# Optimization experiments

Hardware: AMD Instinct MI355X
Metric: run time of the kernel (lower is better)

The kernel has to match this reference:

```python
import jax, jax.numpy as jnp
import numpy as np

D_MODEL = 256
N_LAYER = 8
N_HEAD = 8
D_K = D_MODEL // N_HEAD  # 32
D_FF = 4 * D_MODEL
VOCAB = 5
NUM_BUCKETS = 64
MAX_DIST = 256
L = 768
B = 1
EPS = 1e-5


def _ln(x, s, b):
    m = jnp.mean(x, axis=-1, keepdims=True)
    v = jnp.mean((x - m) ** 2, axis=-1, keepdims=True)
    return (x - m) * jax.lax.rsqrt(v + EPS) * s + b


def _rp_bucket(rel_pos):
    # faithful to RelativePositionBias._relative_position_bucket
    nb = NUM_BUCKETS // 2  # 32
    ret = (rel_pos < 0).astype(jnp.int32) * nb
    arp = jnp.abs(rel_pos)
    max_exact = nb // 2  # 16
    is_small = arp < max_exact
    safe = jnp.maximum(arp, 1).astype(jnp.float32)
    log_ratio = float(np.log(MAX_DIST / max_exact))
    vil = max_exact + (jnp.log(safe / max_exact) / log_ratio * (nb - max_exact)).astype(jnp.int32)
    vil = jnp.minimum(vil, nb - 1)
    return ret + jnp.where(is_small, arp.astype(jnp.int32), vil)


def setup_inputs() -> dict:
    key = jax.random.key(0)
    ks = iter(jax.random.split(key, 40))
    s = 0.02
    d = {}
    d['seq'] = jax.random.randint(next(ks), (B, L), 0, VOCAB, dtype=jnp.int32)
    d['tok_emb'] = jax.random.normal(next(ks), (VOCAB, D_MODEL), jnp.float32) * s
    d['rp_emb'] = jax.random.normal(next(ks), (NUM_BUCKETS, N_HEAD), jnp.float32) * s
    # stacked per-layer params [N_LAYER, ...]
    d['wq'] = jax.random.normal(next(ks), (N_LAYER, D_MODEL, D_MODEL), jnp.float32) * s
    d['wk'] = jax.random.normal(next(ks), (N_LAYER, D_MODEL, D_MODEL), jnp.float32) * s
    d['wv'] = jax.random.normal(next(ks), (N_LAYER, D_MODEL, D_MODEL), jnp.float32) * s
    d['wo'] = jax.random.normal(next(ks), (N_LAYER, D_MODEL, D_MODEL), jnp.float32) * s
    d['ln1_s'] = jnp.ones((N_LAYER, D_MODEL), jnp.float32)
    d['ln1_b'] = jnp.zeros((N_LAYER, D_MODEL), jnp.float32)
    d['ln2_s'] = jnp.ones((N_LAYER, D_MODEL), jnp.float32)
    d['ln2_b'] = jnp.zeros((N_LAYER, D_MODEL), jnp.float32)
    d['ffn_w1'] = jax.random.normal(next(ks), (N_LAYER, D_MODEL, D_FF), jnp.float32) * s
    d['ffn_b1'] = jnp.zeros((N_LAYER, D_FF), jnp.float32)
    d['ffn_w2'] = jax.random.normal(next(ks), (N_LAYER, D_FF, D_MODEL), jnp.float32) * s
    d['ffn_b2'] = jnp.zeros((N_LAYER, D_MODEL), jnp.float32)
    d['lnf_s'] = jnp.ones((D_MODEL,), jnp.float32)
    d['lnf_b'] = jnp.zeros((D_MODEL,), jnp.float32)
    d['pair_q_w'] = jax.random.normal(next(ks), (D_MODEL, D_MODEL), jnp.float32) * s
    d['pair_q_b'] = jnp.zeros((D_MODEL,), jnp.float32)
    d['pair_k_w'] = jax.random.normal(next(ks), (D_MODEL, D_MODEL), jnp.float32) * s
    d['pair_k_b'] = jnp.zeros((D_MODEL,), jnp.float32)
    d['pair_rp_emb'] = jax.random.normal(next(ks), (NUM_BUCKETS, D_MODEL), jnp.float32) * s
    d['cls_w1'] = jax.random.normal(next(ks), (D_MODEL, D_MODEL), jnp.float32) * s
    d['cls_b1'] = jnp.zeros((D_MODEL,), jnp.float32)
    d['cls_w2'] = jax.random.normal(next(ks), (D_MODEL, 2), jnp.float32) * s
    d['cls_b2'] = jnp.zeros((2,), jnp.float32)
    return d


def reference(seq, tok_emb, rp_emb, wq, wk, wv, wo, ln1_s, ln1_b, ln2_s, ln2_b,
              ffn_w1, ffn_b1, ffn_w2, ffn_b2, lnf_s, lnf_b,
              pair_q_w, pair_q_b, pair_k_w, pair_k_b, pair_rp_emb,
              cls_w1, cls_b1, cls_w2, cls_b2):
    scale = D_K ** 0.5
    x = tok_emb[seq]  # [B, L, D]
    pos = jnp.arange(L)
    rel = pos[:, None] - pos[None, :]  # [L, L]
    bucket = _rp_bucket(rel)  # [L, L] int32
    bias = jnp.transpose(rp_emb[bucket], (2, 0, 1))[None]  # [1, H, L, L]

    def step(x, p):
        Wq, Wk, Wv, Wo, s1, b1, s2, b2, fw1, fb1, fw2, fb2 = p
        h = _ln(x, s1, b1)
        q = (h @ Wq).reshape(B, L, N_HEAD, D_K).transpose(0, 2, 1, 3)
        k = (h @ Wk).reshape(B, L, N_HEAD, D_K).transpose(0, 2, 1, 3)
        v = (h @ Wv).reshape(B, L, N_HEAD, D_K).transpose(0, 2, 1, 3)
        attn = jnp.einsum('bhid,bhjd->bhij', q / scale, k) + bias
        attn = jax.nn.softmax(attn, axis=-1)
        o = jnp.einsum('bhij,bhjd->bhid', attn, v)
        o = o.transpose(0, 2, 1, 3).reshape(B, L, D_MODEL) @ Wo
        x = x + o
        h2 = _ln(x, s2, b2)
        f = jax.nn.gelu(h2 @ fw1 + fb1, approximate=False) @ fw2 + fb2
        return x + f, None

    x, _ = jax.lax.scan(step, x, (wq, wk, wv, wo, ln1_s, ln1_b, ln2_s, ln2_b,
                                  ffn_w1, ffn_b1, ffn_w2, ffn_b2))
    x = _ln(x, lnf_s, lnf_b)
    q = x @ pair_q_w + pair_q_b  # [B, L, D]
    k = x @ pair_k_w + pair_k_b
    px = jnp.einsum('bic,bjc->bijc', q, k)  # [B, L, L, D]
    px = px + pair_rp_emb[bucket][None]  # add [L, L, D] pair rel-pos embedding
    px = jax.nn.relu(px @ cls_w1 + cls_b1) @ cls_w2 + cls_b2  # [B, L, L, 2]
    return px
```

## Files before the change

kernel.cpp:

```cpp
#include <hip/hip_runtime.h>
#include <hip/hip_bf16.h>
#include <stdint.h>

#define LSEQ 768
#define DM   256
#define NH   8
#define DK   32
#define DFF  1024
#define NLAYER 8
#define NDD  1535

typedef __attribute__((ext_vector_type(8))) short     bf16x8;
typedef __attribute__((ext_vector_type(8))) _Float16  f16x8;
typedef __attribute__((ext_vector_type(4))) float     f32x4;

__device__ __forceinline__ unsigned short f2bf(float f) {
  unsigned u = __float_as_uint(f);
  u += 0x7fffu + ((u >> 16) & 1u);
  return (unsigned short)(u >> 16);
}
__device__ __forceinline__ unsigned short f2h(float f) {
  union { _Float16 h; unsigned short s; } c;
  c.h = (_Float16)f;
  return c.s;
}
__device__ __forceinline__ unsigned pk2(float a, float b) {
  __hip_bfloat162 h = __float22bfloat162_rn(make_float2(a, b));
  union { __hip_bfloat162 h; unsigned u; } c; c.h = h;
  return c.u;
}
__device__ __forceinline__ int bucket_of(int dd) {
  int rel = dd - 767;
  int ret = rel < 0 ? 32 : 0;
  int arp = rel < 0 ? -rel : rel;
  if (arp < 16) return ret + arp;
  const float lr = 2.772588722239781f;
  float val = logf((float)arp * 0.0625f) / lr * 16.0f;
  int vi = 16 + (int)val;
  return ret + (vi < 31 ? vi : 31);
}

__device__ __forceinline__ void pack8h(unsigned short* dst, int id,
                                       const float* src, int N, int G) {
  int lane = (id >> 3) & 63;
  int rem = id >> 9;
  int g = rem % G, kc = rem / G;
  int kb = kc * 32 + ((lane >> 4) << 3);
  int n = g * 16 + (lane & 15);
  union { unsigned short s[8]; uint4 v; } U;
  #pragma unroll
  for (int e = 0; e < 8; ++e) U.s[e] = f2h(src[(size_t)(kb + e) * N + n]);
  *(uint4*)(dst + id) = U.v;
}

__device__ __forceinline__ void pack8h_cat(unsigned short* dst, int id,
                                           const float* s0, const float* s1,
                                           const float* s2, int G) {
  int lane = (id >> 3) & 63;
  int rem = id >> 9;
  int g = rem % G, kc = rem / G;
  int kb = kc * 32 + ((lane >> 4) << 3);
  int n = g * 16 + (lane & 15);
  const float* sp = n < 256 ? s0 : (n < 512 ? s1 : s2);
  int nn = n & 255;
  union { unsigned short s[8]; uint4 v; } U;
  #pragma unroll
  for (int e = 0; e < 8; ++e) U.s[e] = f2h(sp[(size_t)(kb + e) * 256 + nn]);
  *(uint4*)(dst + id) = U.v;
}

template <int LN, int GR>
__device__ void gemm_tile(const float* gsrc, const int* seqIdx,
                          const float* B, const float* bias, float* C,
                          const float* lns, const float* lnb,
                          int M, int K, int N, int m0, int n0, char* smc) {
  float (*As)[32][68] = (float (*)[32][68])smc;
  float (*Bs)[32][68] = (float (*)[32][68])(smc + 17408);
  float (*stat)[2]    = (float (*)[2])(smc + 34816);
  float (*red)[8]     = (float (*)[8])(smc + 35328);

  int t = threadIdx.x;
  int arow = t >> 2, akq = (t & 3) * 8;
  int mg = m0 + arow;
  int mgc = mg < M ? mg : M - 1;
  const float* Ar = (GR == 1) ? (gsrc + (size_t)seqIdx[mgc] * K)
                              : (gsrc + (size_t)bucket_of(mgc) * K);
  float mean = 0.f, rstd = 0.f;
  if (LN) {
    int lq = t & 3;
    float s = 0.f, s2 = 0.f;
    const float* p = Ar + lq * 64;
    #pragma unroll
    for (int c = 0; c < 64; c += 4) {
      float4 v = *(const float4*)(p + c);
      s  += v.x + v.y + v.z + v.w;
      s2 += v.x * v.x + v.y * v.y + v.z * v.z + v.w * v.w;
    }
    red[arow][lq] = s; red[arow][lq + 4] = s2;
    __syncthreads();
    if (lq == 0) {
      float sm = red[arow][0] + red[arow][1] + red[arow][2] + red[arow][3];
      float sq = red[arow][4] + red[arow][5] + red[arow][6] + red[arow][7];
      float m = sm * (1.f / 256.f);
      float v = sq * (1.f / 256.f) - m * m;
      stat[arow][0] = m;
      stat[arow][1] = rsqrtf(v + 1e-5f);
    }
    __syncthreads();
    mean = stat[arow][0]; rstd = stat[arow][1];
  }

  int bkr = t >> 3, bn8 = (t & 7) * 8;
  int ty = t >> 4, tx = t & 15;
  float acc[4][4] = {};
  int nk = K >> 5;

  for (int kt = 0; kt < nk; ++kt) {
    int k0 = kt << 5;
    float4 a0 = *(const float4*)(Ar + k0 + akq);
    float4 a1 = *(const float4*)(Ar + k0 + akq + 4);
    if (LN) {
      float4 ls0 = *(const float4*)(lns + k0 + akq), ls1 = *(const float4*)(lns + k0 + akq + 4);
      float4 lb0 = *(const float4*)(lnb + k0 + akq), lb1 = *(const float4*)(lnb + k0 + akq + 4);
      a0.x=(a0.x-mean)*rstd*ls0.x+lb0.x; a0.y=(a0.y-mean)*rstd*ls0.y+lb0.y;
      a0.z=(a0.z-mean)*rstd*ls0.z+lb0.z; a0.w=(a0.w-mean)*rstd*ls0.w+lb0.w;
      a1.x=(a1.x-mean)*rstd*ls1.x+lb1.x; a1.y=(a1.y-mean)*rstd*ls1.y+lb1.y;
      a1.z=(a1.z-mean)*rstd*ls1.z+lb1.z; a1.w=(a1.w-mean)*rstd*ls1.w+lb1.w;
    }
    int cur = kt & 1;
    As[cur][akq+0][arow]=a0.x; As[cur][akq+1][arow]=a0.y; As[cur][akq+2][arow]=a0.z; As[cur][akq+3][arow]=a0.w;
    As[cur][akq+4][arow]=a1.x; As[cur][akq+5][arow]=a1.y; As[cur][akq+6][arow]=a1.z; As[cur][akq+7][arow]=a1.w;
    *(float4*)&Bs[cur][bkr][bn8] = *(const float4*)(B + (size_t)(k0 + bkr) * N + n0 + bn8);
    *(float4*)&Bs[cur][bkr][bn8+4] = *(const float4*)(B + (size_t)(k0 + bkr) * N + n0 + bn8 + 4);
    __syncthreads();
    #pragma unroll 8
    for (int kk = 0; kk < 32; ++kk) {
      float4 a = *(float4*)&As[cur][kk][ty * 4];
      float4 b = *(float4*)&Bs[cur][kk][tx * 4];
      acc[0][0]=fmaf(a.x,b.x,acc[0][0]); acc[0][1]=fmaf(a.x,b.y,acc[0][1]);
      acc[0][2]=fmaf(a.x,b.z,acc[0][2]); acc[0][3]=fmaf(a.x,b.w,acc[0][3]);
      acc[1][0]=fmaf(a.y,b.x,acc[1][0]); acc[1][1]=fmaf(a.y,b.y,acc[1][1]);
      acc[1][2]=fmaf(a.y,b.z,acc[1][2]); acc[1][3]=fmaf(a.y,b.w,acc[1][3]);
      acc[2][0]=fmaf(a.z,b.x,acc[2][0]); acc[2][1]=fmaf(a.z,b.y,acc[2][1]);
      acc[2][2]=fmaf(a.z,b.z,acc[2][2]); acc[2][3]=fmaf(a.z,b.w,acc[2][3]);
      acc[3][0]=fmaf(a.w,b.x,acc[3][0]); acc[3][1]=fmaf(a.w,b.y,acc[3][1]);
      acc[3][2]=fmaf(a.w,b.z,acc[3][2]); acc[3][3]=fmaf(a.w,b.w,acc[3][3]);
    }
    __syncthreads();
  }

  #pragma unroll
  for (int u = 0; u < 4; ++u) {
    int m = m0 + ty * 4 + u;
    if (m < M) {
      int n = n0 + tx * 4;
      float4 val = make_float4(acc[u][0], acc[u][1], acc[u][2], acc[u][3]);
      if (bias) {
        float4 bv = *(const float4*)(bias + n);
        val.x += bv.x; val.y += bv.y; val.z += bv.z; val.w += bv.w;
      }
      *(float4*)(C + (size_t)m * N + n) = val;
    }
  }
}

__global__ __launch_bounds__(256, 2) void k_prep(
    const int* __restrict__ seq, const float* __restrict__ tok_emb,
    const float* __restrict__ rp_emb,
    const float* __restrict__ wq, const float* __restrict__ wk,
    const float* __restrict__ wv, const float* __restrict__ wo,
    const float* __restrict__ ffn_w1, const float* __restrict__ ffn_w2,
    const float* __restrict__ ln1s0, const float* __restrict__ ln1b0,
    const float* __restrict__ pair_rp, const float* __restrict__ cls_w1,
    const float* __restrict__ cls_b1,
    const float* __restrict__ pair_q_w, const float* __restrict__ pair_k_w,
    float* x0, float* q0, float* k0, float* v0, float* RB,
    unsigned short* W1p, float* abias,
    unsigned short* Wop, unsigned short* W1pk, unsigned short* W2pk,
    unsigned short* Wqkvp, unsigned short* Wpairp) {
  __shared__ __align__(16) char sm[37376];
  int b = blockIdx.x, t = threadIdx.x;
  if (b < 96) {
    int m0 = (b % 24) * 64, n0 = (b / 24) * 64;
    gemm_tile<0,2>(pair_rp, nullptr, cls_w1, cls_b1, RB,
                   nullptr, nullptr, NDD, 256, 256, m0, n0, sm);
  } else if (b < 240) {
    int u = b - 96;
    int n0g = (u % 12) * 64, m0 = (u / 12) * 64;
    int bi = n0g >> 8, n0 = n0g & 255;
    const float* B = bi == 0 ? wq : (bi == 1 ? wk : wv);
    float* C = bi == 0 ? q0 : (bi == 1 ? k0 : v0);
    gemm_tile<1,1>(tok_emb, seq, B, nullptr, C,
                   ln1s0, ln1b0, LSEQ, 256, 256, m0, n0, sm);
  } else if (b < 432) {
    int row = (b - 240) * 4 + (t >> 6), c = (t & 63) * 4;
    *(float4*)(x0 + (size_t)row * DM + c) =
        *(const float4*)(tok_emb + (size_t)seq[row] * DM + c);
  } else if (b < 438) {
    int dd = (b - 432) * 256 + t;
    if (dd < NDD) {
      int bk = bucket_of(dd);
      #pragma unroll
      for (int h = 0; h < NH; ++h) abias[dd * 8 + h] = rp_emb[bk * 8 + h];
    }
  } else if (b < 502) {
    int base = (b - 438) * 1024 + t * 4;
    #pragma unroll
    for (int uu = 0; uu < 4; ++uu) {
      int id = base + uu;
      int e = id & 7, lane = (id >> 3) & 63, g = (id >> 9) & 15, kc = id >> 13;
      int kg = kc * 32 + (lane >> 4) * 8 + e;
      int n  = g * 16 + (lane & 15);
      W1p[id] = f2bf(cls_w1[(size_t)kg * 256 + n]);
    }
  } else {
    int u = (b - 502) * 2048 + t * 8;
    if (u < 524288) {
      int layer = u >> 16, id = u & 65535;
      pack8h(Wop + ((size_t)layer << 16), id, wo + ((size_t)layer << 16), 256, 16);
    } else if (u < 2621440) {
      int v2 = u - 524288; int layer = v2 >> 18, id = v2 & 262143;
      pack8h(W1pk + ((size_t)layer << 18), id, ffn_w1 + ((size_t)layer << 18), 1024, 64);
    } else if (u < 4718592) {
      int v2 = u - 2621440; int layer = v2 >> 18, id = v2 & 262143;
      pack8h(W2pk + ((size_t)layer << 18), id, ffn_w2 + ((size_t)layer << 18), 256, 16);
    } else if (u < 6291456) {
      int v2 = u - 4718592; int layer = v2 / 196608, id = v2 - layer * 196608;
      pack8h_cat(Wqkvp + (size_t)layer * 196608, id,
                 wq + ((size_t)layer << 16), wk + ((size_t)layer << 16),
                 wv + ((size_t)layer << 16), 48);
    } else {
      int id = u - 6291456;
      pack8h_cat(Wpairp, id, pair_q_w, pair_k_w, pair_k_w, 32);
    }
  }
}

#define ATTN_SMEM 72960

__global__ __launch_bounds__(256, 2) void k_attn2(
    const float* __restrict__ q, const float* __restrict__ k,
    const float* __restrict__ v, const float* __restrict__ abias,
    float* __restrict__ o) {
  extern __shared__ char sm[];
  float* S  = (float*)sm;
  float* KV = (float*)(sm + 49664);
  float* QS = (float*)(sm + 66560);
  float* BS = (float*)(sm + 68672);
  float (*red)[16] = (float (*)[16])(sm + 71808);
  float* mrow = (float*)(sm + 72832);
  float* linv = (float*)(sm + 72896);

  int i0 = blockIdx.x * 16, h = blockIdx.y, hc = h * DK;
  int t = threadIdx.x;

  for (int u = t; u < 783; u += 256)
    BS[u] = abias[(size_t)(i0 + u) * 8 + h];
  {
    int r = t >> 4, c = t & 15;
    const float inv = 0.17677669529663687f;
    QS[r * 33 + c]      = q[(size_t)(i0 + r) * DM + hc + c] * inv;
    QS[r * 33 + c + 16] = q[(size_t)(i0 + r) * DM + hc + c + 16] * inv;
  }

  int kx = t & 31, ry = t >> 5;
  int key = t >> 1, half = t & 1;

  for (int cc = 0; cc < 6; ++cc) {
    const float* kp = k + (size_t)(cc * 128 + key) * DM + hc + half * 16;
    float4 L0 = *(const float4*)(kp);
    float4 L1 = *(const float4*)(kp + 4);
    float4 L2 = *(const float4*)(kp + 8);
    float4 L3 = *(const float4*)(kp + 12);
    __syncthreads();
    int cb = half * 16;
    KV[(cb+ 0)*132+key]=L0.x; KV[(cb+ 1)*132+key]=L0.y; KV[(cb+ 2)*132+key]=L0.z; KV[(cb+ 3)*132+key]=L0.w;
    KV[(cb+ 4)*132+key]=L1.x; KV[(cb+ 5)*132+key]=L1.y; KV[(cb+ 6)*132+key]=L1.z; KV[(cb+ 7)*132+key]=L1.w;
    KV[(cb+ 8)*132+key]=L2.x; KV[(cb+ 9)*132+key]=L2.y; KV[(cb+10)*132+key]=L2.z; KV[(cb+11)*132+key]=L2.w;
    KV[(cb+12)*132+key]=L3.x; KV[(cb+13)*132+key]=L3.y; KV[(cb+14)*132+key]=L3.z; KV[(cb+15)*132+key]=L3.w;
    __syncthreads();

    float s0x=0,s0y=0,s0z=0,s0w=0, s1x=0,s1y=0,s1z=0,s1w=0;
    #pragma unroll
    for (int kk = 0; kk < 32; ++kk) {
      float q0 = QS[(ry*2    )*33 + kk];
      float q1 = QS[(ry*2 + 1)*33 + kk];
      float4 kv4 = *(const float4*)&KV[kk*132 + kx*4];
      s0x = fmaf(q0, kv4.x, s0x); s0y = fmaf(q0, kv4.y, s0y);
      s0z = fmaf(q0, kv4.z, s0z); s0w = fmaf(q0, kv4.w, s0w);
      s1x = fmaf(q1, kv4.x, s1x); s1y = fmaf(q1, kv4.y, s1y);
      s1z = fmaf(q1, kv4.z, s1z); s1w = fmaf(q1, kv4.w, s1w);
    }
    int jb = cc * 128 + kx * 4;
    int r0 = ry * 2, r1 = r0 + 1;
    S[r0*776 + jb+0] = s0x + BS[r0 + 767 - (jb+0)];
    S[r0*776 + jb+1] = s0y + BS[r0 + 767 - (jb+1)];
    S[r0*776 + jb+2] = s0z + BS[r0 + 767 - (jb+2)];
    S[r0*776 + jb+3] = s0w + BS[r0 + 767 - (jb+3)];
    S[r1*776 + jb+0] = s1x + BS[r1 + 767 - (jb+0)];
    S[r1*776 + jb+1] = s1y + BS[r1 + 767 - (jb+1)];
    S[r1*776 + jb+2] = s1z + BS[r1 + 767 - (jb+2)];
    S[r1*776 + jb+3] = s1w + BS[r1 + 767 - (jb+3)];
  }
  __syncthreads();

  {
    int ti = t >> 4, tj = t & 15;
    float mx = -1e30f;
    for (int jc = 0; jc < 48; ++jc)
      mx = fmaxf(mx, S[ti*776 + jc*16 + tj]);
    red[ti][tj] = mx;
    __syncthreads();
    if (tj == 0) {
      float m2 = red[ti][0];
      #pragma unroll
      for (int u = 1; u < 16; ++u) m2 = fmaxf(m2, red[ti][u]);
      mrow[ti] = m2;
    }
    __syncthreads();
    float m2 = mrow[ti];
    float sum = 0.f;
    for (int jc = 0; jc < 48; ++jc) {
      int j = jc*16 + tj;
      float e = __expf(S[ti*776 + j] - m2);
      S[ti*776 + j] = e;
      sum += e;
    }
    red[ti][tj] = sum;
    __syncthreads();
    if (tj == 0) {
      float s2 = 0.f;
      #pragma unroll
      for (int u = 0; u < 16; ++u) s2 += red[ti][u];
      linv[ti] = 1.f / s2;
    }
  }

  int cp = t & 15, jg = t >> 4;
  int c0 = cp * 2, c1 = c0 + 1;
  float oc0[16] = {}, oc1[16] = {};
  for (int cc = 0; cc < 6; ++cc) {
    const float* vp = v + (size_t)(cc * 128 + key) * DM + hc + half * 16;
    float4 L0 = *(const float4*)(vp);
    float4 L1 = *(const float4*)(vp + 4);
    float4 L2 = *(const float4*)(vp + 8);
    float4 L3 = *(const float4*)(vp + 12);
    __syncthreads();
    int cb = half * 16;
    KV[(cb+ 0)*132+key]=L0.x; KV[(cb+ 1)*132+key]=L0.y; KV[(cb+ 2)*132+key]=L0.z; KV[(cb+ 3)*132+key]=L0.w;
    KV[(cb+ 4)*132+key]=L1.x; KV[(cb+ 5)*132+key]=L1.y; KV[(cb+ 6)*132+key]=L1.z; KV[(cb+ 7)*132+key]=L1.w;
    KV[(cb+ 8)*132+key]=L2.x; KV[(cb+ 9)*132+key]=L2.y; KV[(cb+10)*132+key]=L2.z; KV[(cb+11)*132+key]=L2.w;
    KV[(cb+12)*132+key]=L3.x; KV[(cb+13)*132+key]=L3.y; KV[(cb+14)*132+key]=L3.z; KV[(cb+15)*132+key]=L3.w;
    __syncthreads();

    #pragma unroll
    for (int jj2 = 0; jj2 < 2; ++jj2) {
      int jb = jg * 8 + jj2 * 4;
      float4 vA = *(const float4*)&KV[c0*132 + jb];
      float4 vB = *(const float4*)&KV[c1*132 + jb];
      #pragma unroll
      for (int r = 0; r < 16; ++r) {
        float4 sv = *(const float4*)&S[r*776 + cc*128 + jb];
        oc0[r] += sv.x*vA.x + sv.y*vA.y + sv.z*vA.z + sv.w*vA.w;
        oc1[r] += sv.x*vB.x + sv.y*vB.y + sv.z*vB.z + sv.w*vB.w;
      }
    }
  }

  #pragma unroll
  for (int h2 = 0; h2 < 2; ++h2) {
    __syncthreads();
    #pragma unroll
    for (int r = 0; r < 8; ++r) {
      KV[(jg*8 + r)*32 + c0] = oc0[h2*8 + r];
      KV[(jg*8 + r)*32 + c1] = oc1[h2*8 + r];
    }
    __syncthreads();
    int r = t >> 5, c = t & 31;
    float s = 0.f;
    #pragma unroll
    for (int jgg = 0; jgg < 16; ++jgg) s += KV[(jgg*8 + r)*32 + c];
    o[(size_t)(i0 + h2*8 + r) * DM + hc + c] = s * linv[h2*8 + r];
  }
}


__global__ __launch_bounds__(256, 2) void k_t1(
    const float* __restrict__ o, const float* __restrict__ xin,
    const unsigned short* __restrict__ wop,
    const float* __restrict__ ln2s, const float* __restrict__ ln2b,
    const unsigned short* __restrict__ w1p, const float* __restrict__ fb1,
    float* __restrict__ x1, unsigned short* __restrict__ Fg) {
  __shared__ __align__(16) float    Xf[16][260];
  __shared__ __align__(16) _Float16 Ab[16][264];
  int t = threadIdx.x;
  int i0 = blockIdx.x * 16;
  int by = blockIdx.y;
  int w = t >> 6, l = t & 63;
  int lr = l & 15, lq = l >> 4;

  {
    int r = t >> 4, j = t & 15;
    #pragma unroll
    for (int q = 0; q < 4; ++q) {
      int c = j * 4 + q * 64;
      float4 v = *(const float4*)(o + (size_t)(i0 + r) * DM + c);
      union { _Float16 h[4]; uint2 u; } cv;
      cv.h[0] = (_Float16)v.x; cv.h[1] = (_Float16)v.y;
      cv.h[2] = (_Float16)v.z; cv.h[3] = (_Float16)v.w;
      *(uint2*)&Ab[r][c] = cv.u;
      *(float4*)&Xf[r][c] = *(const float4*)(xin + (size_t)(i0 + r) * DM + c);
    }
  }
  __syncthreads();

  f16x8 af[8];
  #pragma unroll
  for (int kc = 0; kc < 8; ++kc)
    af[kc] = *(const f16x8*)&Ab[lr][kc * 32 + lq * 8];

  {
    const unsigned short* wp = wop + (size_t)l * 8;
    #pragma unroll
    for (int gi = 0; gi < 4; ++gi) {
      int g = w * 4 + gi;
      f32x4 ac = {0.f, 0.f, 0.f, 0.f};
      #pragma unroll
      for (int kc = 0; kc < 8; ++kc) {
        f16x8 bb = *(const f16x8*)(wp + ((kc * 16 + g) << 9));
        ac = __builtin_amdgcn_mfma_f32_16x16x32_f16(af[kc], bb, ac, 0, 0, 0);
      }
      int n = g * 16 + lr;
      #pragma unroll
      for (int r = 0; r < 4; ++r)
        Xf[lq * 4 + r][n] += ac[r];
    }
  }
  __syncthreads();

  if (by == 0) {
    int r = t >> 4, j = t & 15;
    #pragma unroll
    for (int q = 0; q < 4; ++q) {
      int c = j * 4 + q * 64;
      *(float4*)(x1 + (size_t)(i0 + r) * DM + c) = *(const float4*)&Xf[r][c];
    }
  }

  {
    int r = t >> 4, j = t & 15;
    int c0 = j * 16;
    float xv[16]; float s1 = 0.f, s2 = 0.f;
    #pragma unroll
    for (int u = 0; u < 16; ++u) {
      xv[u] = Xf[r][c0 + u];
      s1 += xv[u]; s2 += xv[u] * xv[u];
    }
    #pragma unroll
    for (int m = 1; m < 16; m <<= 1) {
      s1 += __shfl_xor(s1, m);
      s2 += __shfl_xor(s2, m);
    }
    float mean = s1 * (1.f / 256.f);
    float var  = s2 * (1.f / 256.f) - mean * mean;
    float rs = rsqrtf(var + 1e-5f);
    #pragma unroll
    for (int p = 0; p < 4; ++p) {
      union { _Float16 h[4]; uint2 u; } cv;
      #pragma unroll
      for (int e = 0; e < 4; ++e) {
        int c = c0 + p * 4 + e;
        cv.h[e] = (_Float16)((xv[p * 4 + e] - mean) * rs * ln2s[c] + ln2b[c]);
      }
      *(uint2*)&Ab[r][c0 + p * 4] = cv.u;
    }
  }
  __syncthreads();

  #pragma unroll
  for (int kc = 0; kc < 8; ++kc)
    af[kc] = *(const f16x8*)&Ab[lr][kc * 32 + lq * 8];

  {
    const unsigned short* wp = w1p + (size_t)l * 8;
    #pragma unroll
    for (int gi = 0; gi < 4; ++gi) {
      int g = by * 16 + w * 4 + gi;
      f32x4 ac = {0.f, 0.f, 0.f, 0.f};
      #pragma unroll
      for (int kc = 0; kc < 8; ++kc) {
        f16x8 bb = *(const f16x8*)(wp + ((kc * 64 + g) << 9));
        ac = __builtin_amdgcn_mfma_f32_16x16x32_f16(af[kc], bb, ac, 0, 0, 0);
      }
      int n = g * 16 + lr;
      float b1 = fb1[n];
      #pragma unroll
      for (int r = 0; r < 4; ++r) {
        float v = ac[r] + b1;
        v = 0.5f * v * (1.f + erff(v * 0.70710678118654752f));
        Fg[(size_t)(i0 + lq * 4 + r) * DFF + n] = f2h(v);
      }
    }
  }
}

__global__ __launch_bounds__(256, 2) void k_t2(
    const unsigned short* __restrict__ Fg, const float* __restrict__ x1,
    const unsigned short* __restrict__ w2p, const float* __restrict__ fb2,
    float* __restrict__ x2) {
  __shared__ __align__(16) _Float16 Fs[16][1032];
  int t = threadIdx.x;
  int i0 = blockIdx.x * 16;
  int by = blockIdx.y;
  int w = t >> 6, l = t & 63;
  int lr = l & 15, lq = l >> 4;

  {
    int r = t >> 4, j = t & 15;
    #pragma unroll
    for (int q = 0; q < 8; ++q) {
      int c = j * 8 + q * 128;
      *(uint4*)&Fs[r][c] = *(const uint4*)(Fg + (size_t)(i0 + r) * DFF + c);
    }
  }
  __syncthreads();

  int g = by * 4 + w;
  const unsigned short* wp = w2p + (size_t)l * 8;
  f32x4 ac0 = {0.f, 0.f, 0.f, 0.f}, ac1 = {0.f, 0.f, 0.f, 0.f};
  #pragma unroll
  for (int kc = 0; kc < 32; kc += 2) {
    f16x8 fa0 = *(const f16x8*)&Fs[lr][kc * 32 + lq * 8];
    f16x8 bb0 = *(const f16x8*)(wp + ((kc * 16 + g) << 9));
    ac0 = __builtin_amdgcn_mfma_f32_16x16x32_f16(fa0, bb0, ac0, 0, 0, 0);
    f16x8 fa1 = *(const f16x8*)&Fs[lr][(kc + 1) * 32 + lq * 8];
    f16x8 bb1 = *(const f16x8*)(wp + (((kc + 1) * 16 + g) << 9));
    ac1 = __builtin_amdgcn_mfma_f32_16x16x32_f16(fa1, bb1, ac1, 0, 0, 0);
  }
  int n = g * 16 + lr;
  float b2v = fb2[n];
  #pragma unroll
  for (int r = 0; r < 4; ++r) {
    int row = i0 + lq * 4 + r;
    x2[(size_t)row * DM + n] =
        x1[(size_t)row * DM + n] + ac0[r] + ac1[r] + b2v;
  }
}

template <int LAST>
__global__ __launch_bounds__(256, 2) void k_t3(
    const float* __restrict__ x2,
    const float* __restrict__ lns, const float* __restrict__ lnb,
    const unsigned short* __restrict__ wnp,
    const float* __restrict__ nb0, const float* __restrict__ nb1,
    float* __restrict__ qo, float* __restrict__ ko, float* __restrict__ vo) {
  __shared__ __align__(16) _Float16 Ab[16][264];
  int t = threadIdx.x;
  int i0 = blockIdx.x * 16;
  int by = blockIdx.y;
  int w = t >> 6, l = t & 63;
  int lr = l & 15, lq = l >> 4;

  {
    int r = t >> 4, j = t & 15;
    int c0 = j * 16;
    const float* xp = x2 + (size_t)(i0 + r) * DM + c0;
    float xv[16]; float s1 = 0.f, s2 = 0.f;
    #pragma unroll
    for (int u = 0; u < 16; u += 4) {
      float4 v = *(const float4*)(xp + u);
      xv[u] = v.x; xv[u+1] = v.y; xv[u+2] = v.z; xv[u+3] = v.w;
      s1 += v.x + v.y + v.z + v.w;
      s2 += v.x*v.x + v.y*v.y + v.z*v.z + v.w*v.w;
    }
    #pragma unroll
    for (int m = 1; m < 16; m <<= 1) {
      s1 += __shfl_xor(s1, m);
      s2 += __shfl_xor(s2, m);
    }
    float mean = s1 * (1.f / 256.f);
    float var  = s2 * (1.f / 256.f) - mean * mean;
    float rs = rsqrtf(var + 1e-5f);
    #pragma unroll
    for (int p = 0; p < 4; ++p) {
      union { _Float16 h[4]; uint2 u; } cv;
      #pragma unroll
      for (int e = 0; e < 4; ++e) {
        int c = c0 + p * 4 + e;
        cv.h[e] = (_Float16)((xv[p * 4 + e] - mean) * rs * lns[c] + lnb[c]);
      }
      *(uint2*)&Ab[r][c0 + p * 4] = cv.u;
    }
  }
  __syncthreads();

  f16x8 af[8];
  #pragma unroll
  for (int kc = 0; kc < 8; ++kc)
    af[kc] = *(const f16x8*)&Ab[lr][kc * 32 + lq * 8];

  const unsigned short* wp = wnp + (size_t)l * 8;
  if (!LAST) {
    #pragma unroll
    for (int gi = 0; gi < 3; ++gi) {
      int g = by * 12 + w * 3 + gi;
      f32x4 ac = {0.f, 0.f, 0.f, 0.f};
      #pragma unroll
      for (int kc = 0; kc < 8; ++kc) {
        f16x8 bb = *(const f16x8*)(wp + ((kc * 48 + g) << 9));
        ac = __builtin_amdgcn_mfma_f32_16x16x32_f16(af[kc], bb, ac, 0, 0, 0);
      }
      int n = g * 16 + lr;
      float* dst = n < 256 ? qo : (n < 512 ? ko : vo);
      int nn = n & 255;
      #pragma unroll
      for (int r = 0; r < 4; ++r)
        dst[(size_t)(i0 + lq * 4 + r) * DM + nn] = ac[r];
    }
  } else {
    #pragma unroll
    for (int gi = 0; gi < 2; ++gi) {
      int g = by * 8 + w * 2 + gi;
      f32x4 ac = {0.f, 0.f, 0.f, 0.f};
      #pragma unroll
      for (int kc = 0; kc < 8; ++kc) {
        f16x8 bb = *(const f16x8*)(wp + ((kc * 32 + g) << 9));
        ac = __builtin_amdgcn_mfma_f32_16x16x32_f16(af[kc], bb, ac, 0, 0, 0);
      }
      int n = g * 16 + lr;
      float* dst = n < 256 ? qo : ko;
      const float* bias = n < 256 ? nb0 : nb1;
      int nn = n & 255;
      float bv = bias[nn];
      #pragma unroll
      for (int r = 0; r < 4; ++r)
        dst[(size_t)(i0 + lq * 4 + r) * DM + nn] = ac[r] + bv;
    }
  }
}

#define PAIR_SMEM 74864

__global__ __launch_bounds__(256, 2) void k_pair(
    const float* __restrict__ pq, const float* __restrict__ pk,
    const unsigned short* __restrict__ W1p, const float* __restrict__ RB,
    const float* __restrict__ w2, const float* __restrict__ b2,
    float* __restrict__ out) {
  extern __shared__ char smem[];
  float* qs   = (float*)smem;
  float* ks   = (float*)(smem + 4160);
  float* RB_s = (float*)(smem + 37440);
  float* racc = (float*)(smem + 73840);

  int t = threadIdx.x;
  int j0 = blockIdx.x * 32;
  int i0 = blockIdx.y * 4;
  int w = t >> 6, l = t & 63;
  int q4 = l >> 4, l15 = l & 15;
  int mwv = w & 1, nwv = w >> 1;

  {
    int row = t >> 6, c4 = (t & 63) * 4;
    *(float4*)(qs + row * 260 + c4) = *(const float4*)(pq + (size_t)(i0 + row) * DM + c4);
    #pragma unroll
    for (int r8 = 0; r8 < 8; ++r8) {
      int idx = t + r8 * 256;
      int kr = idx >> 6, kc4 = (idx & 63) * 4;
      *(float4*)(ks + kr * 260 + kc4) = *(const float4*)(pk + (size_t)(j0 + kr) * DM + kc4);
    }
    int ddmin = i0 - j0 + 736;
    for (int idx = t; idx < 35 * 64; idx += 256) {
      int lc = idx >> 6, c4b = (idx & 63) * 4;
      *(float4*)(RB_s + lc * 260 + c4b) =
          *(const float4*)(RB + (size_t)(ddmin + lc) * 256 + c4b);
    }
    racc[t] = 0.f;
  }
  __syncthreads();

  const unsigned short* Bp = W1p + (size_t)(nwv * 8) * 512 + (size_t)l * 8;
  const float* q0p = qs + (mwv * 2) * 260;
  const float* q1p = qs + (mwv * 2 + 1) * 260;
  const float* k0p = ks + l15 * 260;
  const float* k1p = ks + (16 + l15) * 260;

  f32x4 acc[4][8];
  #pragma unroll
  for (int aa = 0; aa < 4; ++aa)
    #pragma unroll
    for (int bb = 0; bb < 8; ++bb) acc[aa][bb] = (f32x4){0.f, 0.f, 0.f, 0.f};

  bf16x8 bcur[8];
  #pragma unroll
  for (int nt = 0; nt < 8; ++nt) bcur[nt] = *(const bf16x8*)(Bp + nt * 512);

  for (int kc = 0; kc < 8; ++kc) {
    bf16x8 bnxt[8];
    if (kc < 7) {
      const unsigned short* bbn = Bp + (size_t)(kc + 1) * 8192;
      #pragma unroll
      for (int nt = 0; nt < 8; ++nt) bnxt[nt] = *(const bf16x8*)(bbn + nt * 512);
    }
    int c = kc * 32 + q4 * 8;
    float4 qa0 = *(const float4*)(q0p + c), qa1 = *(const float4*)(q0p + c + 4);
    float4 qb0 = *(const float4*)(q1p + c), qb1 = *(const float4*)(q1p + c + 4);
    float4 ka0 = *(const float4*)(k0p + c), ka1 = *(const float4*)(k0p + c + 4);
    float4 kb0 = *(const float4*)(k1p + c), kb1 = *(const float4*)(k1p + c + 4);

    union { bf16x8 v; unsigned u[4]; } af[4];
    af[0].u[0] = pk2(qa0.x*ka0.x, qa0.y*ka0.y); af[0].u[1] = pk2(qa0.z*ka0.z, qa0.w*ka0.w);
    af[0].u[2] = pk2(qa1.x*ka1.x, qa1.y*ka1.y); af[0].u[3] = pk2(qa1.z*ka1.z, qa1.w*ka1.w);
    af[1].u[0] = pk2(qa0.x*kb0.x, qa0.y*kb0.y); af[1].u[1] = pk2(qa0.z*kb0.z, qa0.w*kb0.w);
    af[1].u[2] = pk2(qa1.x*kb1.x, qa1.y*kb1.y); af[1].u[3] = pk2(qa1.z*kb1.z, qa1.w*kb1.w);
    af[2].u[0] = pk2(qb0.x*ka0.x, qb0.y*ka0.y); af[2].u[1] = pk2(qb0.z*ka0.z, qb0.w*ka0.w);
    af[2].u[2] = pk2(qb1.x*ka1.x, qb1.y*ka1.y); af[2].u[3] = pk2(qb1.z*ka1.z, qb1.w*ka1.w);
    af[3].u[0] = pk2(qb0.x*kb0.x, qb0.y*kb0.y); af[3].u[1] = pk2(qb0.z*kb0.z, qb0.w*kb0.w);
    af[3].u[2] = pk2(qb1.x*kb1.x, qb1.y*kb1.y); af[3].u[3] = pk2(qb1.z*kb1.z, qb1.w*kb1.w);

    #pragma unroll
    for (int mt = 0; mt < 4; ++mt)
      #pragma unroll
      for (int nt = 0; nt < 8; ++nt)
        acc[mt][nt] = __builtin_amdgcn_mfma_f32_16x16x32_bf16(af[mt].v, bcur[nt], acc[mt][nt], 0, 0, 0);
    if (kc < 7) {
      #pragma unroll
      for (int nt = 0; nt < 8; ++nt) bcur[nt] = bnxt[nt];
    }
  }

  float w20[8], w21[8];
  #pragma unroll
  for (int nt = 0; nt < 8; ++nt) {
    int n = nwv * 128 + nt * 16 + l15;
    w20[nt] = w2[n * 2];
    w21[nt] = w2[n * 2 + 1];
  }
  #pragma unroll
  for (int mt = 0; mt < 4; ++mt) {
    #pragma unroll
    for (int reg = 0; reg < 4; ++reg) {
      int r = mwv * 64 + mt * 16 + q4 * 4 + reg;
      int lc = (r >> 5) - (r & 31) + 31;
      float o0 = 0.f, o1 = 0.f;
      #pragma unroll
      for (int nt = 0; nt < 8; ++nt) {
        int n = nwv * 128 + nt * 16 + l15;
        float T = acc[mt][nt][reg] + RB_s[lc * 260 + n];
        T = fmaxf(T, 0.f);
        o0 = fmaf(T, w20[nt], o0);
        o1 = fmaf(T, w21[nt], o1);
      }
      #pragma unroll
      for (int s = 1; s < 16; s <<= 1) {
        o0 += __shfl_xor(o0, s);
        o1 += __shfl_xor(o1, s);
      }
      if (l15 == 0) {
        atomicAdd(&racc[r * 2 + 0], o0);
        atomicAdd(&racc[r * 2 + 1], o1);
      }
    }
  }
  __syncthreads();
  {
    int r = t >> 1, oo = t & 1;
    out[((size_t)(i0 + (r >> 5)) * LSEQ + (j0 + (r & 31))) * 2 + oo] = racc[t] + b2[oo];
  }
}

extern "C" void kernel_launch(void* const* d_in, const int* in_sizes, int n_in,
                              void* d_out, int out_size, void* d_ws, size_t ws_size,
                              hipStream_t stream) {
  const int*   seq      = (const int*)  d_in[0];
  const float* tok_emb  = (const float*)d_in[1];
  const float* rp_emb   = (const float*)d_in[2];
  const float* wq       = (const float*)d_in[3];
  const float* wk       = (const float*)d_in[4];
  const float* wv       = (const float*)d_in[5];
  const float* wo       = (const float*)d_in[6];
  const float* ln1_s    = (const float*)d_in[7];
  const float* ln1_b    = (const float*)d_in[8];
  const float* ln2_s    = (const float*)d_in[9];
  const float* ln2_b    = (const float*)d_in[10];
  const float* ffn_w1   = (const float*)d_in[11];
  const float* ffn_b1   = (const float*)d_in[12];
  const float* ffn_w2   = (const float*)d_in[13];
  const float* ffn_b2   = (const float*)d_in[14];
  const float* lnf_s    = (const float*)d_in[15];
  const float* lnf_b    = (const float*)d_in[16];
  const float* pair_q_w = (const float*)d_in[17];
  const float* pair_q_b = (const float*)d_in[18];
  const float* pair_k_w = (const float*)d_in[19];
  const float* pair_k_b = (const float*)d_in[20];
  const float* pair_rp  = (const float*)d_in[21];
  const float* cls_w1   = (const float*)d_in[22];
  const float* cls_b1   = (const float*)d_in[23];
  const float* cls_w2   = (const float*)d_in[24];
  const float* cls_b2   = (const float*)d_in[25];
  float* out = (float*)d_out;

  char* ws = (char*)d_ws;
  float* xb0 = (float*)(ws + 0);
  float* xb1 = (float*)(ws + 786432);
  float* qb[2] = { (float*)(ws + 1572864), (float*)(ws + 3932160) };
  float* kb[2] = { (float*)(ws + 2359296), (float*)(ws + 4718592) };
  float* vb[2] = { (float*)(ws + 3145728), (float*)(ws + 5505024) };
  float* o   = (float*)(ws + 6291456);
  float* pq  = (float*)(ws + 7077888);
  float* pk  = (float*)(ws + 7864320);
  float* RB  = (float*)(ws + 8650752);
  unsigned short* W1p = (unsigned short*)(ws + 10223616);
  float* abias = (float*)(ws + 10354688);
  unsigned short* Wop    = (unsigned short*)(ws + 10403840);
  unsigned short* W1pk   = (unsigned short*)(ws + 11452416);
  unsigned short* W2pk   = (unsigned short*)(ws + 15646720);
  unsigned short* Wqkvp  = (unsigned short*)(ws + 19841024);
  unsigned short* Wpairp = (unsigned short*)(ws + 22986752);
  unsigned short* Fg     = (unsigned short*)(ws + 23248896);
  float* x1buf           = (float*)(ws + 24821760);

  (void)in_sizes; (void)n_in; (void)out_size; (void)ws_size;

  hipFuncSetAttribute(reinterpret_cast<const void*>(k_pair),
                      hipFuncAttributeMaxDynamicSharedMemorySize, PAIR_SMEM);
  hipFuncSetAttribute(reinterpret_cast<const void*>(k_attn2),
                      hipFuncAttributeMaxDynamicSharedMemorySize, ATTN_SMEM);

  k_prep<<<3638, 256, 0, stream>>>(seq, tok_emb, rp_emb, wq, wk, wv, wo,
                                   ffn_w1, ffn_w2, ln1_s, ln1_b,
                                   pair_rp, cls_w1, cls_b1, pair_q_w, pair_k_w,
                                   xb0, qb[0], kb[0], vb[0], RB, W1p, abias,
                                   Wop, W1pk, W2pk, Wqkvp, Wpairp);

  for (int l = 0; l < NLAYER; ++l) {
    int pi = l & 1, po = pi ^ 1;
    float* xin  = (l & 1) ? xb1 : xb0;
    float* xout = (l & 1) ? xb0 : xb1;

    k_attn2<<<dim3(48, 8), 256, ATTN_SMEM, stream>>>(qb[pi], kb[pi], vb[pi], abias, o);

    k_t1<<<dim3(48, 4), 256, 0, stream>>>(
        o, xin, Wop + ((size_t)l << 16),
        ln2_s + l * DM, ln2_b + l * DM,
        W1pk + ((size_t)l << 18), ffn_b1 + (size_t)l * DFF,
        x1buf, Fg);

    k_t2<<<dim3(48, 4), 256, 0, stream>>>(
        Fg, x1buf, W2pk + ((size_t)l << 18), ffn_b2 + (size_t)l * DM, xout);

    if (l < NLAYER - 1) {
      k_t3<0><<<dim3(48, 4), 256, 0, stream>>>(
          xout, ln1_s + (l + 1) * DM, ln1_b + (l + 1) * DM,
          Wqkvp + (size_t)(l + 1) * 196608, nullptr, nullptr,
          qb[po], kb[po], vb[po]);
    } else {
      k_t3<1><<<dim3(48, 4), 256, 0, stream>>>(
          xout, lnf_s, lnf_b, Wpairp, pair_q_b, pair_k_b,
          pq, pk, nullptr);
    }
  }

  k_pair<<<dim3(24, 192), 256, PAIR_SMEM, stream>>>(pq, pk, W1p, RB, cls_w2, cls_b2, out);
}
```

Baseline: 653.1 us.

## Fold query into W1 per row and stream fp16 K tiles in pair head

The pair classifier's first layer is reformulated so each block handles one query row i. It scales W1 by q_i once in registers and runs MFMA on pre-packed fp16 K tiles, double-buffered in shared memory. This removes the per-pair elementwise q*k products, bf16 packing, large shared staging and shared-memory atomics. In exchange it uses fp16 for the q-scaled weights, adds a small K-packing kernel, reads the relative-position table from global memory directly, and synchronises once per tile.

```diff
diff --git a/kernel.cpp b/kernel.cpp
--- a/kernel.cpp
+++ b/kernel.cpp
@@ -23,11 +23,6 @@
   union { _Float16 h; unsigned short s; } c;
   c.h = (_Float16)f;
   return c.s;
-}
-__device__ __forceinline__ unsigned pk2(float a, float b) {
-  __hip_bfloat162 h = __float22bfloat162_rn(make_float2(a, b));
-  union { __hip_bfloat162 h; unsigned u; } c; c.h = h;
-  return c.u;
 }
 __device__ __forceinline__ int bucket_of(int dd) {
   int rel = dd - 767;
@@ -211,7 +206,7 @@
       int e = id & 7, lane = (id >> 3) & 63, g = (id >> 9) & 15, kc = id >> 13;
       int kg = kc * 32 + (lane >> 4) * 8 + e;
       int n  = g * 16 + (lane & 15);
-      W1p[id] = f2bf(cls_w1[(size_t)kg * 256 + n]);
+      W1p[id] = f2h(cls_w1[(size_t)kg * 256 + n]);
     }
   } else {
     int u = (b - 502) * 2048 + t * 8;
@@ -639,132 +634,116 @@
   }
 }
 
-#define PAIR_SMEM 74864
-
-__global__ __launch_bounds__(256, 2) void k_pair(
-    const float* __restrict__ pq, const float* __restrict__ pk,
+__global__ __launch_bounds__(256, 2) void k_kp(
+    const float* __restrict__ pk, unsigned short* __restrict__ Kp) {
+  int fid = blockIdx.x * 256 + threadIdx.x;
+  int jt = fid >> 9;
+  int rem = fid & 511;
+  int kc = rem >> 6, l = rem & 63;
+  int row = jt * 16 + (l & 15);
+  int c = kc * 32 + ((l >> 4) << 3);
+  const float* sp = pk + (size_t)row * DM + c;
+  float4 a = *(const float4*)sp, b = *(const float4*)(sp + 4);
+  f16x8 h;
+  h[0] = (_Float16)a.x; h[1] = (_Float16)a.y; h[2] = (_Float16)a.z; h[3] = (_Float16)a.w;
+  h[4] = (_Float16)b.x; h[5] = (_Float16)b.y; h[6] = (_Float16)b.z; h[7] = (_Float16)b.w;
+  *(f16x8*)(Kp + (size_t)fid * 8) = h;
+}
+
+__global__ __launch_bounds__(512, 2) void k_pair2(
+    const float* __restrict__ pq, const unsigned short* __restrict__ Kp,
     const unsigned short* __restrict__ W1p, const float* __restrict__ RB,
     const float* __restrict__ w2, const float* __restrict__ b2,
     float* __restrict__ out) {
-  extern __shared__ char smem[];
-  float* qs   = (float*)smem;
-  float* ks   = (float*)(smem + 4160);
-  float* RB_s = (float*)(smem + 37440);
-  float* racc = (float*)(smem + 73840);
+  __shared__ __align__(16) _Float16 Ks[2][512][8];
+  __shared__ float qs[256];
+  __shared__ float racc[2][8][16][2];
 
   int t = threadIdx.x;
-  int j0 = blockIdx.x * 32;
-  int i0 = blockIdx.y * 4;
+  int i = blockIdx.x;
   int w = t >> 6, l = t & 63;
-  int q4 = l >> 4, l15 = l & 15;
-  int mwv = w & 1, nwv = w >> 1;
+  int l15 = l & 15, lq = l >> 4;
+  int g0 = w * 2, g1 = g0 + 1;
+  int n0 = g0 * 16 + l15, n1 = g1 * 16 + l15;
 
   {
-    int row = t >> 6, c4 = (t & 63) * 4;
-    *(float4*)(qs + row * 260 + c4) = *(const float4*)(pq + (size_t)(i0 + row) * DM + c4);
-    #pragma unroll
-    for (int r8 = 0; r8 < 8; ++r8) {
-      int idx = t + r8 * 256;
-      int kr = idx >> 6, kc4 = (idx & 63) * 4;
-      *(float4*)(ks + kr * 260 + kc4) = *(const float4*)(pk + (size_t)(j0 + kr) * DM + kc4);
-    }
-    int ddmin = i0 - j0 + 736;
-    for (int idx = t; idx < 35 * 64; idx += 256) {
-      int lc = idx >> 6, c4b = (idx & 63) * 4;
-      *(float4*)(RB_s + lc * 260 + c4b) =
-          *(const float4*)(RB + (size_t)(ddmin + lc) * 256 + c4b);
-    }
-    racc[t] = 0.f;
+    f16x8 k0 = *(const f16x8*)(Kp + (size_t)t * 8);
+    if (t < 64)
+      *(float4*)&qs[t * 4] = *(const float4*)(pq + (size_t)i * DM + t * 4);
+    *(f16x8*)&Ks[0][t][0] = k0;
   }
   __syncthreads();
 
-  const unsigned short* Bp = W1p + (size_t)(nwv * 8) * 512 + (size_t)l * 8;
-  const float* q0p = qs + (mwv * 2) * 260;
-  const float* q1p = qs + (mwv * 2 + 1) * 260;
-  const float* k0p = ks + l15 * 260;
-  const float* k1p = ks + (16 + l15) * 260;
-
-  f32x4 acc[4][8];
-  #pragma unroll
-  for (int aa = 0; aa < 4; ++aa)
-    #pragma unroll
-    for (int bb = 0; bb < 8; ++bb) acc[aa][bb] = (f32x4){0.f, 0.f, 0.f, 0.f};
-
-  bf16x8 bcur[8];
-  #pragma unroll
-  for (int nt = 0; nt < 8; ++nt) bcur[nt] = *(const bf16x8*)(Bp + nt * 512);
-
+  f16x8 bq0[8], bq1[8];
+  #pragma unroll
   for (int kc = 0; kc < 8; ++kc) {
-    bf16x8 bnxt[8];
-    if (kc < 7) {
-      const unsigned short* bbn = Bp + (size_t)(kc + 1) * 8192;
-      #pragma unroll
-      for (int nt = 0; nt < 8; ++nt) bnxt[nt] = *(const bf16x8*)(bbn + nt * 512);
-    }
-    int c = kc * 32 + q4 * 8;
-    float4 qa0 = *(const float4*)(q0p + c), qa1 = *(const float4*)(q0p + c + 4);
-    float4 qb0 = *(const float4*)(q1p + c), qb1 = *(const float4*)(q1p + c + 4);
-    float4 ka0 = *(const float4*)(k0p + c), ka1 = *(const float4*)(k0p + c + 4);
-    float4 kb0 = *(const float4*)(k1p + c), kb1 = *(const float4*)(k1p + c + 4);
-
-    union { bf16x8 v; unsigned u[4]; } af[4];
-    af[0].u[0] = pk2(qa0.x*ka0.x, qa0.y*ka0.y); af[0].u[1] = pk2(qa0.z*ka0.z, qa0.w*ka0.w);
-    af[0].u[2] = pk2(qa1.x*ka1.x, qa1.y*ka1.y); af[0].u[3] = pk2(qa1.z*ka1.z, qa1.w*ka1.w);
-    af[1].u[0] = pk2(qa0.x*kb0.x, qa0.y*kb0.y); af[1].u[1] = pk2(qa0.z*kb0.z, qa0.w*kb0.w);
-    af[1].u[2] = pk2(qa1.x*kb1.x, qa1.y*kb1.y); af[1].u[3] = pk2(qa1.z*kb1.z, qa1.w*kb1.w);
-    af[2].u[0] = pk2(qb0.x*ka0.x, qb0.y*ka0.y); af[2].u[1] = pk2(qb0.z*ka0.z, qb0.w*ka0.w);
-    af[2].u[2] = pk2(qb1.x*ka1.x, qb1.y*ka1.y); af[2].u[3] = pk2(qb1.z*ka1.z, qb1.w*ka1.w);
-    af[3].u[0] = pk2(qb0.x*kb0.x, qb0.y*kb0.y); af[3].u[1] = pk2(qb0.z*kb0.z, qb0.w*kb0.w);
-    af[3].u[2] = pk2(qb1.x*kb1.x, qb1.y*kb1.y); af[3].u[3] = pk2(qb1.z*kb1.z, qb1.w*kb1.w);
-
-    #pragma unroll
-    for (int mt = 0; mt < 4; ++mt)
-      #pragma unroll
-      for (int nt = 0; nt < 8; ++nt)
-        acc[mt][nt] = __builtin_amdgcn_mfma_f32_16x16x32_bf16(af[mt].v, bcur[nt], acc[mt][nt], 0, 0, 0);
-    if (kc < 7) {
-      #pragma unroll
-      for (int nt = 0; nt < 8; ++nt) bcur[nt] = bnxt[nt];
-    }
-  }
-
-  float w20[8], w21[8];
-  #pragma unroll
-  for (int nt = 0; nt < 8; ++nt) {
-    int n = nwv * 128 + nt * 16 + l15;
-    w20[nt] = w2[n * 2];
-    w21[nt] = w2[n * 2 + 1];
-  }
-  #pragma unroll
-  for (int mt = 0; mt < 4; ++mt) {
+    int qb = kc * 32 + lq * 8;
+    float4 qa = *(const float4*)&qs[qb];
+    float4 qbv = *(const float4*)&qs[qb + 4];
+    f16x8 qh;
+    qh[0] = (_Float16)qa.x;  qh[1] = (_Float16)qa.y;
+    qh[2] = (_Float16)qa.z;  qh[3] = (_Float16)qa.w;
+    qh[4] = (_Float16)qbv.x; qh[5] = (_Float16)qbv.y;
+    qh[6] = (_Float16)qbv.z; qh[7] = (_Float16)qbv.w;
+    f16x8 w0 = *(const f16x8*)(W1p + (((size_t)(kc * 16 + g0) * 64 + l) * 8));
+    f16x8 w1 = *(const f16x8*)(W1p + (((size_t)(kc * 16 + g1) * 64 + l) * 8));
+    bq0[kc] = qh * w0;
+    bq1[kc] = qh * w1;
+  }
+
+  float w20a = w2[n0 * 2], w21a = w2[n0 * 2 + 1];
+  float w20b = w2[n1 * 2], w21b = w2[n1 * 2 + 1];
+  float b2v = (t < 32) ? b2[t & 1] : 0.f;
+
+  for (int jt = 0; jt < 48; ++jt) {
+    int buf = jt & 1;
+    f16x8 kreg;
+    if (jt < 47)
+      kreg = *(const f16x8*)(Kp + ((size_t)(jt + 1) * 512 + t) * 8);
+
+    f16x8 afr[8];
+    #pragma unroll
+    for (int kc = 0; kc < 8; ++kc)
+      afr[kc] = *(const f16x8*)&Ks[buf][kc * 64 + l][0];
+
+    f32x4 ac0 = {0.f, 0.f, 0.f, 0.f}, ac1 = {0.f, 0.f, 0.f, 0.f};
+    #pragma unroll
+    for (int kc = 0; kc < 8; ++kc) {
+      ac0 = __builtin_amdgcn_mfma_f32_16x16x32_f16(afr[kc], bq0[kc], ac0, 0, 0, 0);
+      ac1 = __builtin_amdgcn_mfma_f32_16x16x32_f16(afr[kc], bq1[kc], ac1, 0, 0, 0);
+    }
+
+    int jb = jt * 16;
     #pragma unroll
     for (int reg = 0; reg < 4; ++reg) {
-      int r = mwv * 64 + mt * 16 + q4 * 4 + reg;
-      int lc = (r >> 5) - (r & 31) + 31;
-      float o0 = 0.f, o1 = 0.f;
-      #pragma unroll
-      for (int nt = 0; nt < 8; ++nt) {
-        int n = nwv * 128 + nt * 16 + l15;
-        float T = acc[mt][nt][reg] + RB_s[lc * 260 + n];
-        T = fmaxf(T, 0.f);
-        o0 = fmaf(T, w20[nt], o0);
-        o1 = fmaf(T, w21[nt], o1);
-      }
+      int row = lq * 4 + reg;
+      int rbrow = i - (jb + row) + 767;
+      float T0 = fmaxf(ac0[reg] + RB[(size_t)rbrow * 256 + n0], 0.f);
+      float T1 = fmaxf(ac1[reg] + RB[(size_t)rbrow * 256 + n1], 0.f);
+      float p0 = T0 * w20a + T1 * w20b;
+      float p1 = T0 * w21a + T1 * w21b;
       #pragma unroll
       for (int s = 1; s < 16; s <<= 1) {
-        o0 += __shfl_xor(o0, s);
-        o1 += __shfl_xor(o1, s);
+        p0 += __shfl_xor(p0, s);
+        p1 += __shfl_xor(p1, s);
       }
       if (l15 == 0) {
-        atomicAdd(&racc[r * 2 + 0], o0);
-        atomicAdd(&racc[r * 2 + 1], o1);
-      }
-    }
-  }
-  __syncthreads();
-  {
-    int r = t >> 1, oo = t & 1;
-    out[((size_t)(i0 + (r >> 5)) * LSEQ + (j0 + (r & 31))) * 2 + oo] = racc[t] + b2[oo];
+        racc[buf][w][row][0] = p0;
+        racc[buf][w][row][1] = p1;
+      }
+    }
+
+    if (jt < 47)
+      *(f16x8*)&Ks[buf ^ 1][t][0] = kreg;
+    __syncthreads();
+
+    if (t < 32) {
+      int row = t >> 1, oo = t & 1;
+      float s = 0.f;
+      #pragma unroll
+      for (int wv = 0; wv < 8; ++wv) s += racc[buf][wv][row][oo];
+      out[((size_t)i * LSEQ + jb + row) * 2 + oo] = s + b2v;
+    }
   }
 }
 
@@ -818,11 +797,10 @@
   unsigned short* Wpairp = (unsigned short*)(ws + 22986752);
   unsigned short* Fg     = (unsigned short*)(ws + 23248896);
   float* x1buf           = (float*)(ws + 24821760);
+  unsigned short* Kp     = (unsigned short*)(ws + 25608192);
 
   (void)in_sizes; (void)n_in; (void)out_size; (void)ws_size;
 
-  hipFuncSetAttribute(reinterpret_cast<const void*>(k_pair),
-                      hipFuncAttributeMaxDynamicSharedMemorySize, PAIR_SMEM);
   hipFuncSetAttribute(reinterpret_cast<const void*>(k_attn2),
                       hipFuncAttributeMaxDynamicSharedMemorySize, ATTN_SMEM);
 
@@ -860,5 +838,6 @@
     }
   }
 
-  k_pair<<<dim3(24, 192), 256, PAIR_SMEM, stream>>>(pq, pk, W1p, RB, cls_w2, cls_b2, out);
-}
+  k_kp<<<96, 256, 0, stream>>>(pk, Kp);
+  k_pair2<<<768, 512, 0, stream>>>(pq, Kp, W1p, RB, cls_w2, cls_b2, out);
+}
```

New measurement: 797.8 us. +22.2%, slower.
